# Performance work log

Hardware: AMD Instinct MI355X
Metric: run time of the kernel (lower is better)

## Reference

```python
import jax, jax.numpy as jnp
import numpy as np
import math

NUM_ROTATIONS = 8
STRIDE = 1
PADDING = 1


def _rotate_weights(weight, num_rotations):
    """Bilinear rotation of conv filters, matching torch affine_grid/grid_sample
    with align_corners=False and zero padding.

    weight: (O, I, k, k) -> returns (R, O, I, k, k)
    """
    O, I, k, _ = weight.shape
    dt = weight.dtype
    # align_corners=False normalized pixel-center coords in [-1, 1]
    c = (2.0 * jnp.arange(k, dtype=jnp.float32) + 1.0) / k - 1.0
    ygrid, xgrid = jnp.meshgrid(c, c, indexing='ij')          # (k, k)
    angles = 2.0 * math.pi * jnp.arange(num_rotations, dtype=jnp.float32) / num_rotations
    cos = jnp.cos(angles)[:, None, None]                       # (R,1,1)
    sin = jnp.sin(angles)[:, None, None]
    # theta = [[cos, -sin, 0], [sin, cos, 0]] applied to (x, y, 1)
    xs = cos * xgrid - sin * ygrid                             # (R,k,k)
    ys = sin * xgrid + cos * ygrid
    # unnormalize (align_corners=False): ix = ((x+1)*W - 1)/2
    ix = ((xs + 1.0) * k - 1.0) * 0.5
    iy = ((ys + 1.0) * k - 1.0) * 0.5
    ix0f = jnp.floor(ix); iy0f = jnp.floor(iy)
    wx1 = (ix - ix0f).astype(dt); wy1 = (iy - iy0f).astype(dt)
    wx0 = 1.0 - wx1; wy0 = 1.0 - wy1
    ix0 = ix0f.astype(jnp.int32); iy0 = iy0f.astype(jnp.int32)
    ix1 = ix0 + 1; iy1 = iy0 + 1

    def gather(iyc, ixc):
        valid = ((iyc >= 0) & (iyc < k) & (ixc >= 0) & (ixc < k)).astype(dt)
        iycl = jnp.clip(iyc, 0, k - 1)
        ixcl = jnp.clip(ixc, 0, k - 1)
        # advanced indexing broadcasts: (O, I, R, k, k)
        return weight[:, :, iycl, ixcl] * valid

    out = (gather(iy0, ix0) * (wy0 * wx0)
           + gather(iy0, ix1) * (wy0 * wx1)
           + gather(iy1, ix0) * (wy1 * wx0)
           + gather(iy1, ix1) * (wy1 * wx1))                   # (O,I,R,k,k)
    return jnp.transpose(out, (2, 0, 1, 3, 4))                 # (R,O,I,k,k)


def setup_inputs() -> dict:
    key = jax.random.key(0)
    k1, k2 = jax.random.split(key)
    x = jax.random.normal(k1, (4, 256, 128, 128), dtype=jnp.float32)
    weight = jax.random.normal(k2, (256, 256, 3, 3), dtype=jnp.float32)
    return {"x": x, "weight": weight}


def reference(x, weight):
    R = NUM_ROTATIONS
    O, I, k, _ = weight.shape
    rw = _rotate_weights(weight, R)                            # (R,O,I,k,k)
    rw_flat = rw.reshape(R * O, I, k, k)
    # one conv for all rotations (same input), then max over rotations
    out = jax.lax.conv_general_dilated(
        x, rw_flat,
        window_strides=(STRIDE, STRIDE),
        padding=[(PADDING, PADDING), (PADDING, PADDING)],
        dimension_numbers=('NCHW', 'OIHW', 'NCHW'))           # (B, R*O, H', W')
    B, _, Hp, Wp = out.shape
    out = out.reshape(B, R, O, Hp, Wp)
    return jnp.max(out, axis=1)                                # (B, O, H', W')
```

## Files before the change

kernel.cpp:

```cpp
#include <hip/hip_runtime.h>
#include <hip/hip_bf16.h>
#include <math.h>

typedef __attribute__((ext_vector_type(8))) short bf16x8;
typedef __attribute__((ext_vector_type(16))) float f32x16;

#define R_TOTAL 8
#define CIN     256
#define COUT    256
#define HH      128
#define WW      128
#define BB      4
#define MTOT    (COUT * R_TOTAL)
#define KTAPS   9

#define ROWSZ 4160
#define ABUF  (128 * 32)

__device__ __forceinline__ void g2l16(void* lds, const void* g) {
    __builtin_amdgcn_global_load_lds(
        (const __attribute__((address_space(1))) unsigned int*)g,
        (__attribute__((address_space(3))) unsigned int*)lds,
        16, 0, 0);
}

__global__ __launch_bounds__(256)
void to_nhwc_bf16(const float* __restrict__ x, __hip_bfloat16* __restrict__ xb) {
    __shared__ __hip_bfloat16 t[32][33];
    const int b  = blockIdx.z;
    const int c0 = blockIdx.y * 32;
    const int p0 = blockIdx.x * 32;
    const int tx = threadIdx.x & 31;
    const int ty = threadIdx.x >> 5;
    const float* xp = x + (size_t)b * CIN * (HH * WW);
    #pragma unroll
    for (int j = 0; j < 4; ++j) {
        int c = ty * 4 + j;
        t[c][tx] = __float2bfloat16(xp[(size_t)(c0 + c) * (HH * WW) + p0 + tx]);
    }
    __syncthreads();
    __hip_bfloat16* op = xb + ((size_t)b * (HH * WW) + p0) * CIN + c0;
    #pragma unroll
    for (int j = 0; j < 4; ++j) {
        int p = ty * 4 + j;
        op[(size_t)p * CIN + tx] = t[tx][p];
    }
}

__global__ __launch_bounds__(256)
void zero_guard_row(__hip_bfloat16* __restrict__ xb) {
    size_t base = (size_t)BB * HH * WW * CIN;
    int i = blockIdx.x * 256 + threadIdx.x;
    xb[base + i] = __float2bfloat16(0.0f);
}

__global__ __launch_bounds__(256)
void rotate_weights_bf16(const float* __restrict__ w, __hip_bfloat16* __restrict__ rwb) {
    const int i = threadIdx.x;
    const int m = blockIdx.x;
    const int o = m >> 3, r = m & 7;

    float ang = 6.283185307179586f * (float)r / 8.0f;
    float cs = cosf(ang), sn = sinf(ang);

    const float* wp = w + ((size_t)o * CIN + i) * 9;
    __hip_bfloat16* op = rwb + (size_t)m * (KTAPS * CIN) + i;

    #pragma unroll
    for (int ky = 0; ky < 3; ++ky) {
        #pragma unroll
        for (int kx = 0; kx < 3; ++kx) {
            float yg = (2.0f * (float)ky + 1.0f) / 3.0f - 1.0f;
            float xg = (2.0f * (float)kx + 1.0f) / 3.0f - 1.0f;
            float xsf = cs * xg - sn * yg;
            float ysf = sn * xg + cs * yg;
            float ix = ((xsf + 1.0f) * 3.0f - 1.0f) * 0.5f;
            float iy = ((ysf + 1.0f) * 3.0f - 1.0f) * 0.5f;
            float ix0f = floorf(ix), iy0f = floorf(iy);
            float wx1 = ix - ix0f,  wy1 = iy - iy0f;
            float wx0 = 1.0f - wx1, wy0 = 1.0f - wy1;
            int ix0 = (int)ix0f, iy0 = (int)iy0f;
            int ix1 = ix0 + 1,   iy1 = iy0 + 1;
            float acc = 0.0f;
            if (iy0 >= 0 && iy0 < 3 && ix0 >= 0 && ix0 < 3) acc += wp[iy0*3+ix0] * (wy0*wx0);
            if (iy0 >= 0 && iy0 < 3 && ix1 >= 0 && ix1 < 3) acc += wp[iy0*3+ix1] * (wy0*wx1);
            if (iy1 >= 0 && iy1 < 3 && ix0 >= 0 && ix0 < 3) acc += wp[iy1*3+ix0] * (wy1*wx0);
            if (iy1 >= 0 && iy1 < 3 && ix1 >= 0 && ix1 < 3) acc += wp[iy1*3+ix1] * (wy1*wx1);
            op[(ky * 3 + kx) * CIN] = __float2bfloat16(acc);
        }
    }
}

__global__ __launch_bounds__(256, 2)
void rotconv_mfma_kernel(const __hip_bfloat16* __restrict__ xb,
                         const __hip_bfloat16* __restrict__ rwb,
                         float* __restrict__ out) {
    const int tid  = threadIdx.x;
    const int lane = tid & 63;
    const int w    = tid >> 6;
    const int wm   = w >> 1;
    const int wn   = w & 1;
    const int l31  = lane & 31;
    const int lh   = lane >> 5;

    const int bid = (blockIdx.x & 7) * 512 + (blockIdx.x >> 3);
    const int mt  = bid >> 8;
    const int nt  = bid & 255;
    const int b   = nt >> 6;
    const int y0  = (nt & 63) * 2;
    const int m0  = mt << 7;

    __shared__ __align__(16) __hip_bfloat16 xs[5 * ROWSZ];
    __shared__ __align__(16) __hip_bfloat16 As[4 * ABUF];

    for (int j = tid; j < 5 * 64; j += 256) {
        int slot = j >> 6;
        int rem  = j & 63;
        int colL = (rem >> 5) ? 129 : 0;
        int ch   = rem & 31;
        xs[slot * ROWSZ + colL * 32 + ch] = __float2bfloat16(0.0f);
    }

    const int arow_r = wm * 64 + l31;
    const int aswz   = (arow_r >> 1) & 3;
    const int aOffS0 = arow_r * 32 + 8 * ((lh)     ^ aswz);
    const int aOffS1 = arow_r * 32 + 8 * ((lh + 2) ^ aswz);
    int bOffS[3][2];
    #pragma unroll
    for (int kx = 0; kx < 3; ++kx) {
        int colL = l31 + kx;
        int swz  = (colL >> 1) & 3;
        bOffS[kx][0] = colL * 32 + 8 * ((lh)     ^ swz);
        bOffS[kx][1] = colL * 32 + 8 * ((lh + 2) ^ swz);
    }

    const int arow0 = w * 32 + (lane >> 2);
    const int arow1 = arow0 + 16;
    const int dstA0 = (w * 32) * 32;
    const int dstA1 = (w * 32 + 16) * 32;
    const int voffA0 = (m0 + arow0) * (KTAPS * CIN) + 8 * ((lane & 3) ^ ((arow0 >> 1) & 3));
    const int voffA1 = (m0 + arow1) * (KTAPS * CIN) + 8 * ((lane & 3) ^ ((arow1 >> 1) & 3));

    int rowOff[4];
    #pragma unroll
    for (int r = 0; r < 4; ++r) {
        int gy = y0 - 1 + r;
        int rowIdx = ((unsigned)gy < (unsigned)HH) ? (b * HH + gy) : (BB * HH);
        rowOff[r] = rowIdx * (WW * CIN);
    }
    const int gx0   = w * 16 + (lane >> 2);
    const int voffX = gx0 * CIN + 8 * ((lane & 3) ^ (((gx0 + 1) >> 1) & 3));
    const int dstXp0 = 32 + w * 512;
    const int dstXp1 = 32 + (w + 4) * 512;

    f32x16 acc[2][4];
    #pragma unroll
    for (int mi = 0; mi < 2; ++mi)
        #pragma unroll
        for (int ni = 0; ni < 4; ++ni)
            #pragma unroll
            for (int e = 0; e < 16; ++e)
                acc[mi][ni][e] = 0.0f;

    __syncthreads();

    #pragma unroll
    for (int r = 0; r < 4; ++r) {
        g2l16(xs + r * ROWSZ + dstXp0, xb + rowOff[r] + voffX);
        g2l16(xs + r * ROWSZ + dstXp1, xb + rowOff[r] + voffX + 64 * CIN);
    }
    g2l16(As + dstA0, rwb + voffA0);
    g2l16(As + dstA1, rwb + voffA1);
    g2l16(As + ABUF + dstA0, rwb + voffA0 + CIN);
    g2l16(As + ABUF + dstA1, rwb + voffA1 + CIN);
    asm volatile("s_waitcnt vmcnt(0)" ::: "memory");
    __syncthreads();

#define WRAP5(v) ((v) >= 5 ? (v) - 5 : (v))

#define TAP(C, P, NW, DOA, DOX, XIDX, XSLOT, XOFF)                             \
  {                                                                            \
    if (DOA) {                                                                 \
      __hip_bfloat16* ab = As + (((C) + (P) + 2) & 3) * ABUF;                  \
      const int aofs = (((P) + 2) % 9) * CIN + ((((P) + 2) / 9) + (C)) * 32;   \
      g2l16(ab + dstA0, rwb + voffA0 + aofs);                                  \
      g2l16(ab + dstA1, rwb + voffA1 + aofs);                                  \
    }                                                                          \
    if (DOX) {                                                                 \
      g2l16(xs + (XSLOT) * ROWSZ + (((XIDX) & 1) ? dstXp1 : dstXp0),           \
            xb + rowOff[(XIDX) >> 1] + voffX + ((XIDX) & 1) * (64 * CIN)       \
               + (XOFF));                                                      \
    }                                                                          \
    asm volatile("s_waitcnt vmcnt(%0)" :: "i"(NW) : "memory");                 \
    asm volatile("s_barrier" ::: "memory");                                    \
    {                                                                          \
      const __hip_bfloat16* ar = As + (((C) + (P)) & 3) * ABUF;                \
      const __hip_bfloat16* br =                                               \
          ((P) / 3 == 0 ? xrow0 : (P) / 3 == 1 ? xrow1 : xrow2);               \
      _Pragma("unroll")                                                        \
      for (int s = 0; s < 2; ++s) {                                            \
        const int ao = s ? aOffS1 : aOffS0;                                    \
        const int bo = bOffS[(P) % 3][s];                                      \
        bf16x8 a0 = *(const bf16x8*)(ar + ao);                                 \
        bf16x8 a1 = *(const bf16x8*)(ar + ao + 1024);                          \
        bf16x8 b0 = *(const bf16x8*)(br + bo);                                 \
        bf16x8 b1 = *(const bf16x8*)(br + bo + 1024);                          \
        bf16x8 b2 = *(const bf16x8*)(br + bo + 2048);                          \
        bf16x8 b3 = *(const bf16x8*)(br + bo + 3072);                          \
        __builtin_amdgcn_s_setprio(1);                                         \
        acc[0][0] = __builtin_amdgcn_mfma_f32_32x32x16_bf16(a0, b0, acc[0][0], 0, 0, 0); \
        acc[0][1] = __builtin_amdgcn_mfma_f32_32x32x16_bf16(a0, b1, acc[0][1], 0, 0, 0); \
        acc[0][2] = __builtin_amdgcn_mfma_f32_32x32x16_bf16(a0, b2, acc[0][2], 0, 0, 0); \
        acc[0][3] = __builtin_amdgcn_mfma_f32_32x32x16_bf16(a0, b3, acc[0][3], 0, 0, 0); \
        acc[1][0] = __builtin_amdgcn_mfma_f32_32x32x16_bf16(a1, b0, acc[1][0], 0, 0, 0); \
        acc[1][1] = __builtin_amdgcn_mfma_f32_32x32x16_bf16(a1, b1, acc[1][1], 0, 0, 0); \
        acc[1][2] = __builtin_amdgcn_mfma_f32_32x32x16_bf16(a1, b2, acc[1][2], 0, 0, 0); \
        acc[1][3] = __builtin_amdgcn_mfma_f32_32x32x16_bf16(a1, b3, acc[1][3], 0, 0, 0); \
        __builtin_amdgcn_s_setprio(0);                                         \
      }                                                                        \
    }                                                                          \
  }

#define CHUNK_HDR(C)                                                           \
    const int rbw = ((4 * (C)) % 5) + wn;                                      \
    const __hip_bfloat16* xrow0 = xs + WRAP5(rbw) * ROWSZ;                     \
    const __hip_bfloat16* xrow1 = xs + WRAP5(rbw + 1) * ROWSZ;                 \
    const __hip_bfloat16* xrow2 = xs + WRAP5(rbw + 2) * ROWSZ;

#define CHK_MID(C)                                                             \
  { CHUNK_HDR(C)                                                               \
    TAP(C, 0, 6, 1, 0, 0, 0, 0)                                                \
    TAP(C, 1, 6, 1, 1, 6, (4*(C)+3)%5, (C)*32)                                 \
    TAP(C, 2, 6, 1, 1, 7, (4*(C)+3)%5, (C)*32)                                 \
    TAP(C, 3, 7, 1, 1, 0, (4*(C)+4)%5, ((C)+1)*32)                             \
    TAP(C, 4, 7, 1, 1, 1, (4*(C)+4)%5, ((C)+1)*32)                             \
    TAP(C, 5, 7, 1, 1, 2, (4*(C))%5,   ((C)+1)*32)                             \
    TAP(C, 6, 7, 1, 1, 3, (4*(C))%5,   ((C)+1)*32)                             \
    TAP(C, 7, 7, 1, 1, 4, (4*(C)+1)%5, ((C)+1)*32)                             \
    TAP(C, 8, 7, 1, 1, 5, (4*(C)+1)%5, ((C)+1)*32)                             \
  }

    { CHUNK_HDR(0)
      TAP(0, 0, 2, 1, 0, 0, 0, 0)
      TAP(0, 1, 4, 1, 0, 0, 0, 0)
      TAP(0, 2, 4, 1, 0, 0, 0, 0)
      TAP(0, 3, 5, 1, 1, 0, 4, 32)
      TAP(0, 4, 6, 1, 1, 1, 4, 32)
      TAP(0, 5, 7, 1, 1, 2, 0, 32)
      TAP(0, 6, 7, 1, 1, 3, 0, 32)
      TAP(0, 7, 7, 1, 1, 4, 1, 32)
      TAP(0, 8, 7, 1, 1, 5, 1, 32)
    }

    CHK_MID(1) CHK_MID(2) CHK_MID(3) CHK_MID(4) CHK_MID(5) CHK_MID(6)

    { CHUNK_HDR(7)
      TAP(7, 0, 6, 1, 0, 0, 0, 0)
      TAP(7, 1, 6, 1, 1, 6, 1, 224)
      TAP(7, 2, 6, 1, 1, 7, 1, 224)
      TAP(7, 3, 6, 1, 0, 0, 0, 0)
      TAP(7, 4, 5, 1, 0, 0, 0, 0)
      TAP(7, 5, 4, 1, 0, 0, 0, 0)
      TAP(7, 6, 4, 1, 0, 0, 0, 0)
      TAP(7, 7, 2, 0, 0, 0, 0, 0)
      TAP(7, 8, 0, 0, 0, 0, 0, 0)
    }

#undef TAP
#undef CHK_MID
#undef CHUNK_HDR
#undef WRAP5

    const int yOut = y0 + wn;
    #pragma unroll
    for (int mi = 0; mi < 2; ++mi) {
        #pragma unroll
        for (int ni = 0; ni < 4; ++ni) {
            #pragma unroll
            for (int g = 0; g < 4; ++g) {
                float v = fmaxf(fmaxf(acc[mi][ni][4*g+0], acc[mi][ni][4*g+1]),
                                fmaxf(acc[mi][ni][4*g+2], acc[mi][ni][4*g+3]));
                v = fmaxf(v, __shfl_xor(v, 32));
                if (lane < 32) {
                    int o = ((m0 + wm * 64 + mi * 32) >> 3) + g;
                    out[(((size_t)(b * COUT + o)) * HH + yOut) * WW
                        + ni * 32 + lane] = v;
                }
            }
        }
    }
}

__global__ void rotate_weights_kernel(const float* __restrict__ w,
                                      float* __restrict__ rw,
                                      int r0, int rcount) {
    int idx = blockIdx.x * blockDim.x + threadIdx.x;
    int total = COUT * CIN * rcount;
    if (idx >= total) return;
    int rr = idx % rcount;
    int ii = (idx / rcount) % CIN;
    int oo = idx / (rcount * CIN);
    int r  = r0 + rr;
    float ang = 6.283185307179586f * (float)r / 8.0f;
    float cs = cosf(ang), sn = sinf(ang);
    const float* wp = w  + ((size_t)oo * CIN + ii) * 9;
    float*       op = rw + (((size_t)oo * CIN + ii) * rcount + rr) * 9;
    #pragma unroll
    for (int ky = 0; ky < 3; ++ky)
        #pragma unroll
        for (int kx = 0; kx < 3; ++kx) {
            float yg = (2.0f * ky + 1.0f) / 3.0f - 1.0f;
            float xg = (2.0f * kx + 1.0f) / 3.0f - 1.0f;
            float xsf = cs * xg - sn * yg;
            float ysf = sn * xg + cs * yg;
            float ix = ((xsf + 1.0f) * 3.0f - 1.0f) * 0.5f;
            float iy = ((ysf + 1.0f) * 3.0f - 1.0f) * 0.5f;
            float ix0f = floorf(ix), iy0f = floorf(iy);
            float wx1 = ix - ix0f,  wy1 = iy - iy0f;
            float wx0 = 1.0f - wx1, wy0 = 1.0f - wy1;
            int ix0 = (int)ix0f, iy0 = (int)iy0f;
            int ix1 = ix0 + 1,   iy1 = iy0 + 1;
            float acc = 0.0f;
            if (iy0 >= 0 && iy0 < 3 && ix0 >= 0 && ix0 < 3) acc += wp[iy0*3+ix0]*(wy0*wx0);
            if (iy0 >= 0 && iy0 < 3 && ix1 >= 0 && ix1 < 3) acc += wp[iy0*3+ix1]*(wy0*wx1);
            if (iy1 >= 0 && iy1 < 3 && ix0 >= 0 && ix0 < 3) acc += wp[iy1*3+ix0]*(wy1*wx0);
            if (iy1 >= 0 && iy1 < 3 && ix1 >= 0 && ix1 < 3) acc += wp[iy1*3+ix1]*(wy1*wx1);
            op[ky * 3 + kx] = acc;
        }
}

template <int RCOUNT>
__global__ __launch_bounds__(256)
void rotconv_max_kernel(const float* __restrict__ x,
                        const float* __restrict__ rw,
                        float* __restrict__ out,
                        int first) {
    const int tid = threadIdx.x;
    const int tx = tid & 15;
    const int ty = tid >> 4;
    const int x0 = blockIdx.x * 32;
    const int y0 = blockIdx.y * 32;
    const int o  = blockIdx.z % COUT;
    const int b  = blockIdx.z / COUT;
    __shared__ float xsm[34][36];
    float acc[RCOUNT][2][2];
    #pragma unroll
    for (int r = 0; r < RCOUNT; ++r)
        #pragma unroll
        for (int py = 0; py < 2; ++py)
            #pragma unroll
            for (int px = 0; px < 2; ++px) acc[r][py][px] = 0.0f;
    for (int i = 0; i < CIN; ++i) {
        __syncthreads();
        const float* xp = x + ((size_t)(b * CIN + i)) * (HH * WW);
        for (int idx = tid; idx < 34 * 34; idx += 256) {
            int row = idx / 34, col = idx - row * 34;
            int gy = y0 - 1 + row, gx = x0 - 1 + col;
            float v = 0.0f;
            if (gy >= 0 && gy < HH && gx >= 0 && gx < WW) v = xp[gy * WW + gx];
            xsm[row][col] = v;
        }
        __syncthreads();
        float xv[4][4];
        #pragma unroll
        for (int ry = 0; ry < 4; ++ry)
            #pragma unroll
            for (int cx = 0; cx < 4; ++cx) xv[ry][cx] = xsm[ty*2+ry][tx*2+cx];
        const float* wp = rw + ((size_t)(o * CIN + i)) * (RCOUNT * 9);
        #pragma unroll
        for (int r = 0; r < RCOUNT; ++r) {
            float wv[9];
            #pragma unroll
            for (int t2 = 0; t2 < 9; ++t2) wv[t2] = wp[r * 9 + t2];
            #pragma unroll
            for (int py = 0; py < 2; ++py)
                #pragma unroll
                for (int px = 0; px < 2; ++px) {
                    float a = acc[r][py][px];
                    #pragma unroll
                    for (int ky = 0; ky < 3; ++ky)
                        #pragma unroll
                        for (int kx = 0; kx < 3; ++kx)
                            a += xv[py+ky][px+kx] * wv[ky*3+kx];
                    acc[r][py][px] = a;
                }
        }
    }
    #pragma unroll
    for (int py = 0; py < 2; ++py)
        #pragma unroll
        for (int px = 0; px < 2; ++px) {
            float m = acc[0][py][px];
            #pragma unroll
            for (int r = 1; r < RCOUNT; ++r) m = fmaxf(m, acc[r][py][px]);
            int oy = y0 + ty * 2 + py;
            int ox = x0 + tx * 2 + px;
            float* op = out + (((size_t)(b * COUT + o)) * HH + oy) * WW + ox;
            if (first) *op = m;
            else       *op = fmaxf(*op, m);
        }
}

extern "C" void kernel_launch(void* const* d_in, const int* in_sizes, int n_in,
                              void* d_out, int out_size, void* d_ws, size_t ws_size,
                              hipStream_t stream) {
    const float* x = (const float*)d_in[0];
    const float* w = (const float*)d_in[1];
    float* out = (float*)d_out;

    const size_t xbBytes = ((size_t)BB * HH * WW + WW) * CIN * sizeof(__hip_bfloat16);
    const size_t rwBytes = (size_t)MTOT * KTAPS * CIN * sizeof(__hip_bfloat16);

    if (ws_size >= xbBytes + rwBytes) {
        __hip_bfloat16* xbuf = (__hip_bfloat16*)d_ws;
        __hip_bfloat16* rwb  = (__hip_bfloat16*)((char*)d_ws + xbBytes);

        to_nhwc_bf16<<<dim3((HH * WW) / 32, CIN / 32, BB), 256, 0, stream>>>(x, xbuf);
        zero_guard_row<<<(WW * CIN) / 256, 256, 0, stream>>>(xbuf);
        rotate_weights_bf16<<<MTOT, 256, 0, stream>>>(w, rwb);
        rotconv_mfma_kernel<<<4096, 256, 0, stream>>>(xbuf, rwb, out);
        return;
    }

    float* rw = (float*)d_ws;
    int chunk = 8;
    while (chunk > 1 && (size_t)COUT * CIN * chunk * 9 * sizeof(float) > ws_size)
        chunk >>= 1;
    int first = 1;
    for (int r0 = 0; r0 < R_TOTAL; r0 += chunk) {
        int rc = chunk;
        int total = COUT * CIN * rc;
        rotate_weights_kernel<<<(total + 255) / 256, 256, 0, stream>>>(w, rw, r0, rc);
        dim3 grid(WW / 32, HH / 32, BB * COUT);
        switch (rc) {
            case 8: rotconv_max_kernel<8><<<grid, 256, 0, stream>>>(x, rw, out, first); break;
            case 4: rotconv_max_kernel<4><<<grid, 256, 0, stream>>>(x, rw, out, first); break;
            case 2: rotconv_max_kernel<2><<<grid, 256, 0, stream>>>(x, rw, out, first); break;
            default: rotconv_max_kernel<1><<<grid, 256, 0, stream>>>(x, rw, out, first); break;
        }
        first = 0;
    }
}
```

Measured before the change: 593.1 us.

## Split LDS tiles into two 16-channel halves instead of XOR-swizzled 32-channel rows

Reorganizes the LDS layout of both the weight tile and the input row buffers. Each 32-channel K-slice is now stored as two contiguous 16-channel halves, replacing the XOR-swizzled 32-wide rows. The global-to-LDS loads, the index precomputation and the MFMA operand reads are rewritten to match. The goal is simpler address arithmetic and possibly fewer LDS bank conflicts, but the new unswizzled stride-16 layout may add conflicts of its own.

```diff
diff --git a/kernel.cpp b/kernel.cpp
--- a/kernel.cpp
+++ b/kernel.cpp
@@ -15,7 +15,9 @@
 #define KTAPS   9
 
 #define ROWSZ 4160
-#define ABUF  (128 * 32)
+#define SHX   2080
+#define ABUF  4096
+#define SHA   2048
 
 __device__ __forceinline__ void g2l16(void* lds, const void* g) {
     __builtin_amdgcn_global_load_lds(
@@ -116,30 +118,21 @@
     for (int j = tid; j < 5 * 64; j += 256) {
         int slot = j >> 6;
         int rem  = j & 63;
-        int colL = (rem >> 5) ? 129 : 0;
-        int ch   = rem & 31;
-        xs[slot * ROWSZ + colL * 32 + ch] = __float2bfloat16(0.0f);
-    }
-
-    const int arow_r = wm * 64 + l31;
-    const int aswz   = (arow_r >> 1) & 3;
-    const int aOffS0 = arow_r * 32 + 8 * ((lh)     ^ aswz);
-    const int aOffS1 = arow_r * 32 + 8 * ((lh + 2) ^ aswz);
-    int bOffS[3][2];
-    #pragma unroll
-    for (int kx = 0; kx < 3; ++kx) {
-        int colL = l31 + kx;
-        int swz  = (colL >> 1) & 3;
-        bOffS[kx][0] = colL * 32 + 8 * ((lh)     ^ swz);
-        bOffS[kx][1] = colL * 32 + 8 * ((lh + 2) ^ swz);
-    }
-
-    const int arow0 = w * 32 + (lane >> 2);
-    const int arow1 = arow0 + 16;
-    const int dstA0 = (w * 32) * 32;
-    const int dstA1 = (w * 32 + 16) * 32;
-    const int voffA0 = (m0 + arow0) * (KTAPS * CIN) + 8 * ((lane & 3) ^ ((arow0 >> 1) & 3));
-    const int voffA1 = (m0 + arow1) * (KTAPS * CIN) + 8 * ((lane & 3) ^ ((arow1 >> 1) & 3));
+        int s    = rem >> 5;
+        int colsel = (rem >> 4) & 1;
+        int e    = rem & 15;
+        int colL = colsel ? 129 : 0;
+        xs[slot * ROWSZ + s * SHX + colL * 16 + e] = __float2bfloat16(0.0f);
+    }
+
+    const int aBase = (wm * 64 + l31) * 16 + lh * 8;
+    int bBase[3];
+    #pragma unroll
+    for (int kx = 0; kx < 3; ++kx)
+        bBase[kx] = (l31 + kx) * 16 + lh * 8;
+
+    const int dstA = w * 512;
+    const int voffA = (m0 + w * 32 + (lane >> 1)) * (KTAPS * CIN) + 8 * (lane & 1);
 
     int rowOff[4];
     #pragma unroll
@@ -148,10 +141,8 @@
         int rowIdx = ((unsigned)gy < (unsigned)HH) ? (b * HH + gy) : (BB * HH);
         rowOff[r] = rowIdx * (WW * CIN);
     }
-    const int gx0   = w * 16 + (lane >> 2);
-    const int voffX = gx0 * CIN + 8 * ((lane & 3) ^ (((gx0 + 1) >> 1) & 3));
-    const int dstXp0 = 32 + w * 512;
-    const int dstXp1 = 32 + (w + 4) * 512;
+    const int voffX = (w * 32 + (lane >> 1)) * CIN + 8 * (lane & 1);
+    const int dstX  = (1 + 32 * w) * 16;
 
     f32x16 acc[2][4];
     #pragma unroll
@@ -166,13 +157,13 @@
 
     #pragma unroll
     for (int r = 0; r < 4; ++r) {
-        g2l16(xs + r * ROWSZ + dstXp0, xb + rowOff[r] + voffX);
-        g2l16(xs + r * ROWSZ + dstXp1, xb + rowOff[r] + voffX + 64 * CIN);
-    }
-    g2l16(As + dstA0, rwb + voffA0);
-    g2l16(As + dstA1, rwb + voffA1);
-    g2l16(As + ABUF + dstA0, rwb + voffA0 + CIN);
-    g2l16(As + ABUF + dstA1, rwb + voffA1 + CIN);
+        g2l16(xs + r * ROWSZ + dstX,       xb + rowOff[r] + voffX);
+        g2l16(xs + r * ROWSZ + SHX + dstX, xb + rowOff[r] + voffX + 16);
+    }
+    g2l16(As + dstA,              rwb + voffA);
+    g2l16(As + SHA + dstA,        rwb + voffA + 16);
+    g2l16(As + ABUF + dstA,       rwb + voffA + CIN);
+    g2l16(As + ABUF + SHA + dstA, rwb + voffA + CIN + 16);
     asm volatile("s_waitcnt vmcnt(0)" ::: "memory");
     __syncthreads();
 
@@ -183,13 +174,13 @@
     if (DOA) {                                                                 \
       __hip_bfloat16* ab = As + (((C) + (P) + 2) & 3) * ABUF;                  \
       const int aofs = (((P) + 2) % 9) * CIN + ((((P) + 2) / 9) + (C)) * 32;   \
-      g2l16(ab + dstA0, rwb + voffA0 + aofs);                                  \
-      g2l16(ab + dstA1, rwb + voffA1 + aofs);                                  \
+      g2l16(ab + dstA,       rwb + voffA + aofs);                              \
+      g2l16(ab + SHA + dstA, rwb + voffA + aofs + 16);                         \
     }                                                                          \
     if (DOX) {                                                                 \
-      g2l16(xs + (XSLOT) * ROWSZ + (((XIDX) & 1) ? dstXp1 : dstXp0),           \
-            xb + rowOff[(XIDX) >> 1] + voffX + ((XIDX) & 1) * (64 * CIN)       \
-               + (XOFF));                                                      \
+      g2l16(xs + (XSLOT) * ROWSZ + (((XIDX) & 1) ? SHX : 0) + dstX,            \
+            xb + rowOff[(XIDX) >> 1] + voffX + (XOFF)                          \
+               + (((XIDX) & 1) ? 16 : 0));                                     \
     }                                                                          \
     asm volatile("s_waitcnt vmcnt(%0)" :: "i"(NW) : "memory");                 \
     asm volatile("s_barrier" ::: "memory");                                    \
@@ -199,14 +190,14 @@
           ((P) / 3 == 0 ? xrow0 : (P) / 3 == 1 ? xrow1 : xrow2);               \
       _Pragma("unroll")                                                        \
       for (int s = 0; s < 2; ++s) {                                            \
-        const int ao = s ? aOffS1 : aOffS0;                                    \
-        const int bo = bOffS[(P) % 3][s];                                      \
-        bf16x8 a0 = *(const bf16x8*)(ar + ao);                                 \
-        bf16x8 a1 = *(const bf16x8*)(ar + ao + 1024);                          \
-        bf16x8 b0 = *(const bf16x8*)(br + bo);                                 \
-        bf16x8 b1 = *(const bf16x8*)(br + bo + 1024);                          \
-        bf16x8 b2 = *(const bf16x8*)(br + bo + 2048);                          \
-        bf16x8 b3 = *(const bf16x8*)(br + bo + 3072);                          \
+        const __hip_bfloat16* as_ = ar + s * SHA + aBase;                      \
+        const __hip_bfloat16* bs_ = br + s * SHX + bBase[(P) % 3];             \
+        bf16x8 a0 = *(const bf16x8*)(as_);                                     \
+        bf16x8 a1 = *(const bf16x8*)(as_ + 512);                               \
+        bf16x8 b0 = *(const bf16x8*)(bs_);                                     \
+        bf16x8 b1 = *(const bf16x8*)(bs_ + 512);                               \
+        bf16x8 b2 = *(const bf16x8*)(bs_ + 1024);                              \
+        bf16x8 b3 = *(const bf16x8*)(bs_ + 1536);                              \
         __builtin_amdgcn_s_setprio(1);                                         \
         acc[0][0] = __builtin_amdgcn_mfma_f32_32x32x16_bf16(a0, b0, acc[0][0], 0, 0, 0); \
         acc[0][1] = __builtin_amdgcn_mfma_f32_32x32x16_bf16(a0, b1, acc[0][1], 0, 0, 0); \
```

After: 608.3 us. 2.6% more time.
